# Kernel tuning notes

Measured on AMD Instinct MI355X. Metric: run time of the kernel, lower is better.

The kernel has to match this reference:

```python
import jax, jax.numpy as jnp
import numpy as np

B, T, C, H = 4, 2048, 1024, 16
D = C // H          # head_dim = 64
FF = 2 * C          # ff_mult = 2
EPS = 1e-5


def _layernorm(x, g, b):
    mu = jnp.mean(x, axis=-1, keepdims=True)
    var = jnp.mean((x - mu) ** 2, axis=-1, keepdims=True)
    return (x - mu) * jax.lax.rsqrt(var + EPS) * g + b


def setup_inputs() -> dict:
    key = jax.random.key(0)
    ks = jax.random.split(key, 8)
    x = jax.random.normal(ks[0], (B, T, C), dtype=jnp.float32)
    perm = jax.random.permutation(ks[1], T).astype(jnp.int32)
    s_c = 1.0 / np.sqrt(C)
    s_f = 1.0 / np.sqrt(FF)
    Wqkv = jax.random.normal(ks[2], (C, 3 * C), dtype=jnp.float32) * s_c
    Wproj = jax.random.normal(ks[3], (C, C), dtype=jnp.float32) * s_c
    bproj = jnp.zeros((C,), dtype=jnp.float32)
    ln1_g = jnp.ones((C,), dtype=jnp.float32)
    ln1_b = jnp.zeros((C,), dtype=jnp.float32)
    ln2_g = jnp.ones((C,), dtype=jnp.float32)
    ln2_b = jnp.zeros((C,), dtype=jnp.float32)
    Wff1 = jax.random.normal(ks[4], (C, FF), dtype=jnp.float32) * s_c
    bff1 = jnp.zeros((FF,), dtype=jnp.float32)
    Wff2 = jax.random.normal(ks[5], (FF, C), dtype=jnp.float32) * s_f
    bff2 = jnp.zeros((C,), dtype=jnp.float32)
    return {"x": x, "perm": perm, "Wqkv": Wqkv, "Wproj": Wproj, "bproj": bproj,
            "ln1_g": ln1_g, "ln1_b": ln1_b, "ln2_g": ln2_g, "ln2_b": ln2_b,
            "Wff1": Wff1, "bff1": bff1, "Wff2": Wff2, "bff2": bff2}


def reference(x, perm, Wqkv, Wproj, bproj, ln1_g, ln1_b, ln2_g, ln2_b,
              Wff1, bff1, Wff2, bff2):
    # --- attention branch ---
    h = _layernorm(x, ln1_g, ln1_b)                       # [B,T,C]
    qkv = (h @ Wqkv).reshape(B, T, 3, H, D)
    q, k, v = qkv[:, :, 0], qkv[:, :, 1], qkv[:, :, 2]    # [B,T,H,D]
    # random-permuted causal additive mask: masked = ~tril[:, perm]
    rows = jnp.arange(T)[:, None]
    masked = perm[None, :] > rows                          # [T,T] bool
    bias = jnp.where(masked, -jnp.inf, 0.0).astype(x.dtype)
    scale = 1.0 / np.sqrt(D)
    scores = jnp.einsum('bqhd,bkhd->bhqk', q, k) * scale + bias
    attn = jax.nn.softmax(scores, axis=-1)                 # [B,H,T,T]
    y = jnp.einsum('bhqk,bkhd->bqhd', attn, v).reshape(B, T, C)
    x = x + y @ Wproj + bproj
    # --- MLP branch ---
    h2 = _layernorm(x, ln2_g, ln2_b)
    ff = jax.nn.gelu(h2 @ Wff1 + bff1, approximate=False) @ Wff2 + bff2
    return x + ff
```

## Files before the change

kernel.cpp:

```cpp
#include <hip/hip_runtime.h>
#include <math.h>

#define Bb 4
#define Tt 2048
#define Cc 1024
#define Hh 16
#define Dd 64
#define FFf 2048
#define Mrows (Bb*Tt)

typedef _Float16 f16;
typedef _Float16 half8 __attribute__((ext_vector_type(8)));
typedef _Float16 half4 __attribute__((ext_vector_type(4)));
typedef _Float16 half2 __attribute__((ext_vector_type(2)));
typedef float floatx4 __attribute__((ext_vector_type(4)));
typedef float floatx16 __attribute__((ext_vector_type(16)));

#define MFMA16(a,b,c)    __builtin_amdgcn_mfma_f32_16x16x32_f16(a,b,c,0,0,0)
#define MFMA16K16(a,b,c) __builtin_amdgcn_mfma_f32_16x16x16f16(a,b,c,0,0,0)
#define MFMA32(a,b,c)    __builtin_amdgcn_mfma_f32_32x32x16_f16(a,b,c,0,0,0)

__device__ __forceinline__ void g2l16(const void* g, void* l) {
  __builtin_amdgcn_global_load_lds((__attribute__((address_space(1))) void*)(g),
                                   (__attribute__((address_space(3))) void*)(l),
                                   16, 0, 0);
}

__global__ __launch_bounds__(256) void wt_ln_kernel(
    const float* __restrict__ Wqkv, const float* __restrict__ Wproj,
    const float* __restrict__ Wff1, const float* __restrict__ Wff2,
    f16* __restrict__ WqkvT, f16* __restrict__ WprojT,
    f16* __restrict__ Wff1T, f16* __restrict__ Wff2T,
    const float* __restrict__ x, const float* __restrict__ gam,
    const float* __restrict__ bet, f16* __restrict__ lnout,
    const int* __restrict__ perm, int* __restrict__ inv) {
  const int tid = threadIdx.x;
  if (blockIdx.x >= 16384) {
    #pragma unroll
    for (int i = tid; i < Tt; i += 256) inv[perm[i]] = i;
    return;
  }
  if (blockIdx.x < 8192) {
    __shared__ float tile[32][33];
    int idx = blockIdx.x;
    const float* W; f16* WT; int K, N, n0, k0;
    if (idx < 3072)      { W = Wqkv;  WT = WqkvT;  K = Cc;  N = 3*Cc; n0 = (idx % 96)*32; k0 = (idx / 96)*32; }
    else if (idx < 4096) { idx -= 3072; W = Wproj; WT = WprojT; K = Cc;  N = Cc;  n0 = (idx % 32)*32; k0 = (idx / 32)*32; }
    else if (idx < 6144) { idx -= 4096; W = Wff1;  WT = Wff1T;  K = Cc;  N = FFf; n0 = (idx % 64)*32; k0 = (idx / 64)*32; }
    else                 { idx -= 6144; W = Wff2;  WT = Wff2T;  K = FFf; N = Cc;  n0 = (idx % 32)*32; k0 = (idx / 32)*32; }
    const int tx = tid & 31, ty = tid >> 5;
    #pragma unroll
    for (int i = 0; i < 4; i++)
      tile[ty + 8*i][tx] = W[(size_t)(k0 + ty + 8*i) * N + n0 + tx];
    __syncthreads();
    #pragma unroll
    for (int i = 0; i < 4; i++)
      WT[(size_t)(n0 + ty + 8*i) * K + k0 + tx] = (f16)tile[tx][ty + 8*i];
  } else {
    const int row = blockIdx.x - 8192;
    const float4 v = ((const float4*)(x + (size_t)row * Cc))[tid];
    float s  = v.x + v.y + v.z + v.w;
    float ss = v.x*v.x + v.y*v.y + v.z*v.z + v.w*v.w;
    #pragma unroll
    for (int o = 32; o >= 1; o >>= 1) { s += __shfl_xor(s, o); ss += __shfl_xor(ss, o); }
    __shared__ float ps[4], pss[4];
    if ((tid & 63) == 0) { ps[tid >> 6] = s; pss[tid >> 6] = ss; }
    __syncthreads();
    s  = ps[0] + ps[1] + ps[2] + ps[3];
    ss = pss[0] + pss[1] + pss[2] + pss[3];
    const float mu   = s * (1.0f / Cc);
    const float rstd = rsqrtf(ss * (1.0f / Cc) - mu * mu + 1e-5f);
    const float4 g4 = ((const float4*)gam)[tid];
    const float4 b4 = ((const float4*)bet)[tid];
    half4 o;
    o[0] = (f16)((v.x - mu) * rstd * g4.x + b4.x);
    o[1] = (f16)((v.y - mu) * rstd * g4.y + b4.y);
    o[2] = (f16)((v.z - mu) * rstd * g4.z + b4.z);
    o[3] = (f16)((v.w - mu) * rstd * g4.w + b4.w);
    ((half4*)(lnout + (size_t)row * Cc))[tid] = o;
  }
}

__global__ __launch_bounds__(256) void ln_kernel(const float* __restrict__ x,
                                                 const float* __restrict__ gam,
                                                 const float* __restrict__ bet,
                                                 f16* __restrict__ out) {
  const int row = blockIdx.x;
  const int tid = threadIdx.x;
  const float4 v = ((const float4*)(x + (size_t)row * Cc))[tid];
  float s  = v.x + v.y + v.z + v.w;
  float ss = v.x*v.x + v.y*v.y + v.z*v.z + v.w*v.w;
  #pragma unroll
  for (int o = 32; o >= 1; o >>= 1) { s += __shfl_xor(s, o); ss += __shfl_xor(ss, o); }
  __shared__ float ps[4], pss[4];
  if ((tid & 63) == 0) { ps[tid >> 6] = s; pss[tid >> 6] = ss; }
  __syncthreads();
  s  = ps[0] + ps[1] + ps[2] + ps[3];
  ss = pss[0] + pss[1] + pss[2] + pss[3];
  const float mu   = s * (1.0f / Cc);
  const float rstd = rsqrtf(ss * (1.0f / Cc) - mu * mu + 1e-5f);
  const float4 g4 = ((const float4*)gam)[tid];
  const float4 b4 = ((const float4*)bet)[tid];
  half4 o;
  o[0] = (f16)((v.x - mu) * rstd * g4.x + b4.x);
  o[1] = (f16)((v.y - mu) * rstd * g4.y + b4.y);
  o[2] = (f16)((v.z - mu) * rstd * g4.z + b4.z);
  o[3] = (f16)((v.w - mu) * rstd * g4.w + b4.w);
  ((half4*)(out + (size_t)row * Cc))[tid] = o;
}

template <int MODE>
__device__ __forceinline__ void gemm_epilogue_tile(
    const floatx16& a, int rowBase, int col, int khalf,
    const float* __restrict__ resid, const float* __restrict__ bias,
    float* __restrict__ outF, f16* __restrict__ outH,
    f16* __restrict__ outQ, f16* __restrict__ outK, f16* __restrict__ outV) {
  if (MODE == 0) {
    const int s = col >> 10;
    const int hh = (col >> 6) & 15;
    const int d = col & 63;
    #pragma unroll
    for (int g = 0; g < 4; g++) {
      const int row0 = rowBase + 4*khalf + 8*g;
      const int bI = row0 >> 11;
      const int t0 = row0 & 2047;
      if (s == 2) {
        const size_t addr = (((size_t)(bI*Hh + hh)) * Dd + d) * Tt +
                            (t0 & ~63) + ((t0 >> 2) & 3)*16 + ((t0 >> 4) & 3)*4;
        half4 o;
        #pragma unroll
        for (int r = 0; r < 4; r++) o[r] = (f16)a[g*4 + r];
        *(half4*)&outV[addr] = o;
      } else {
        f16* dst = (s == 0) ? outQ : outK;
        const float sc = (s == 0) ? 0.18033688f : 1.0f;
        #pragma unroll
        for (int r = 0; r < 4; r++)
          dst[(((size_t)(bI*Hh + hh)) * Tt + t0 + r) * Dd + d] = (f16)(a[g*4 + r] * sc);
      }
    }
  } else {
    #pragma unroll
    for (int g = 0; g < 4; g++) {
      #pragma unroll
      for (int r = 0; r < 4; r++) {
        const int row = rowBase + 4*khalf + 8*g + r;
        const float vv = a[g*4 + r];
        if (MODE == 1) {
          const size_t ad = (size_t)row * Cc + col;
          outF[ad] = vv + resid[ad] + bias[col];
        } else if (MODE == 2) {
          const float t = vv + bias[col];
          const float gl = 0.5f * t * (1.0f + erff(t * 0.70710678118654752f));
          outH[(size_t)row * FFf + col] = (f16)gl;
        } else {
          const size_t ad = (size_t)row * Cc + col;
          outF[ad] = vv + bias[col] + resid[ad];
        }
      }
    }
  }
}

template <int MODE>
__global__ __launch_bounds__(256, 4) void gemm_kernel(
    const f16* __restrict__ A, const f16* __restrict__ Bt, const int Kdim,
    const float* __restrict__ resid, const float* __restrict__ bias,
    float* __restrict__ outF, f16* __restrict__ outH,
    f16* __restrict__ outQ, f16* __restrict__ outK, f16* __restrict__ outV,
    const int* __restrict__ inv) {
  __shared__ f16 As[128 * 64];
  __shared__ f16 Bs[128 * 64];
  const int tid = threadIdx.x;
  const int lane = tid & 63;
  const int w = tid >> 6;
  const int wr = w >> 1, wc = w & 1;

  const int fid = blockIdx.y * gridDim.x + blockIdx.x;
  const int xcd = fid & 7;
  const int s = fid >> 3;
  const int r = s & 63;
  const int bm = xcd * 8 + (r >> 3);
  const int bn = (s >> 6) * 8 + (r & 7);

  floatx16 acc[2][2] = {};

  const int srow = lane >> 3;
  const int scol = ((lane & 7) ^ srow) * 8;
  size_t aRow[4];
  {
    const int r0 = bm*128 + w*32 + srow;
    if (MODE == 0 && bn >= 8) {
      const int bI = r0 >> 11;
      const int t0 = r0 & 2047;
      #pragma unroll
      for (int c = 0; c < 4; c++)
        aRow[c] = (size_t)(bI*Tt + inv[t0 + c*8]) * Kdim + scol;
    } else {
      #pragma unroll
      for (int c = 0; c < 4; c++)
        aRow[c] = (size_t)(r0 + c*8) * Kdim + scol;
    }
  }
  const size_t bBase = (size_t)(bn*128 + w*32 + srow) * Kdim + scol;

  const int m0 = wr*64 + (lane & 31);
  const int n0 = wc*64 + (lane & 31);
  const int khalf = lane >> 5;
  const int mx = (lane & 7);

  for (int ks = 0; ks < Kdim; ks += 64) {
    __syncthreads();
    #pragma unroll
    for (int c = 0; c < 4; c++) {
      g2l16(A  + aRow[c] + ks, &As[(w*32 + c*8) * 64]);
      g2l16(Bt + bBase + (size_t)(c*8)*Kdim + ks, &Bs[(w*32 + c*8) * 64]);
    }
    __syncthreads();
    #pragma unroll
    for (int kk = 0; kk < 4; kk++) {
      const int kg = kk*2 + khalf;
      half8 aF[2], bF[2];
      aF[0] = *(const half8*)&As[(m0     ) * 64 + ((kg ^ mx) * 8)];
      aF[1] = *(const half8*)&As[(m0 + 32) * 64 + ((kg ^ mx) * 8)];
      bF[0] = *(const half8*)&Bs[(n0     ) * 64 + ((kg ^ mx) * 8)];
      bF[1] = *(const half8*)&Bs[(n0 + 32) * 64 + ((kg ^ mx) * 8)];
      acc[0][0] = MFMA32(aF[0], bF[0], acc[0][0]);
      acc[0][1] = MFMA32(aF[0], bF[1], acc[0][1]);
      acc[1][0] = MFMA32(aF[1], bF[0], acc[1][0]);
      acc[1][1] = MFMA32(aF[1], bF[1], acc[1][1]);
    }
  }

  #pragma unroll
  for (int mi = 0; mi < 2; mi++)
    #pragma unroll
    for (int ni = 0; ni < 2; ni++)
      gemm_epilogue_tile<MODE>(acc[mi][ni], bm*128 + wr*64 + mi*32,
                               bn*128 + wc*64 + ni*32 + (lane & 31), khalf,
                               resid, bias, outF, outH, outQ, outK, outV);
}

__global__ __launch_bounds__(256, 4) void attn_kernel(
    const f16* __restrict__ Q, const f16* __restrict__ Kg,
    const f16* __restrict__ Vtp, f16* __restrict__ Y) {
  __shared__ f16 Ks[64 * 64];
  __shared__ f16 Vs[64 * 64];

  const int tid = threadIdx.x;
  const int lane = tid & 63;
  const int w = tid >> 6;
  const int low = lane & 15;
  const int quad = lane >> 4;
  const int bh = blockIdx.x;
  const int y = blockIdx.y;
  const int b = bh >> 4, h = bh & 15;

  const half4 ones4 = {(f16)1.f, (f16)1.f, (f16)1.f, (f16)1.f};
  const int gd = ((lane & 7) ^ (lane >> 3)) * 8;
  const int krow = lane >> 3;

  for (int pi = 0; pi < 2; pi++) {
    const int tile = (pi == 0) ? y : 15 - y;
    const int q0 = tile * 128;

    half8 qF[2][2];
    {
      const size_t base = ((size_t)bh * Tt + q0 + w*32) * Dd;
      #pragma unroll
      for (int qi = 0; qi < 2; qi++)
        #pragma unroll
        for (int kc = 0; kc < 2; kc++)
          qF[qi][kc] = *(const half8*)(Q + base + (size_t)(qi*16 + low) * Dd +
                                       kc*32 + quad*8);
    }

    floatx4 O[4][2] = {};
    floatx4 Ol[2] = {};
    const int nkb = (q0 >> 6) + 2;

    for (int kt = 0; kt < nkb; kt++) {
      const int kbase = kt * 64;
      __syncthreads();
      {
        const size_t kgBase = ((size_t)bh * Tt + kbase) * Dd;
        const size_t vgBase = ((size_t)bh * Dd) * Tt + kbase;
        g2l16(Kg  + kgBase + (size_t)(w*16 + 0 + krow) * Dd + gd, &Ks[(w*2 + 0) * 512]);
        g2l16(Kg  + kgBase + (size_t)(w*16 + 8 + krow) * Dd + gd, &Ks[(w*2 + 1) * 512]);
        g2l16(Vtp + vgBase + (size_t)(w*16 + 0 + krow) * Tt + gd, &Vs[(w*2 + 0) * 512]);
        g2l16(Vtp + vgBase + (size_t)(w*16 + 8 + krow) * Tt + gd, &Vs[(w*2 + 1) * 512]);
      }
      __syncthreads();

      floatx4 S[2][4] = {};
      #pragma unroll
      for (int kc = 0; kc < 2; kc++) {
        #pragma unroll
        for (int ki = 0; ki < 4; ki++) {
          const int key = ki*16 + low;
          const half8 kf = *(const half8*)&Ks[key * 64 + (((kc*4 + quad) ^ (lane & 7)) * 8)];
          S[0][ki] = MFMA16(kf, qF[0][kc], S[0][ki]);
          S[1][ki] = MFMA16(kf, qF[1][kc], S[1][ki]);
        }
      }

      half4 pF[2][4];
      const bool needmask = (kbase + 63 > q0 + w*32);
      if (needmask) {
        #pragma unroll
        for (int qi = 0; qi < 2; qi++) {
          const int qrow = q0 + w*32 + qi*16 + low;
          #pragma unroll
          for (int ki = 0; ki < 4; ki++) {
            const floatx4 sv = S[qi][ki];
            const int kj = kbase + ki*16 + quad*4;
            const float p0 = (kj + 0 > qrow) ? 0.f : __builtin_amdgcn_exp2f(sv[0]);
            const float p1 = (kj + 1 > qrow) ? 0.f : __builtin_amdgcn_exp2f(sv[1]);
            const float p2 = (kj + 2 > qrow) ? 0.f : __builtin_amdgcn_exp2f(sv[2]);
            const float p3 = (kj + 3 > qrow) ? 0.f : __builtin_amdgcn_exp2f(sv[3]);
            const half2 lo = __builtin_bit_cast(half2, __builtin_amdgcn_cvt_pkrtz(p0, p1));
            const half2 hi = __builtin_bit_cast(half2, __builtin_amdgcn_cvt_pkrtz(p2, p3));
            pF[qi][ki] = __builtin_shufflevector(lo, hi, 0, 1, 2, 3);
          }
        }
      } else {
        #pragma unroll
        for (int qi = 0; qi < 2; qi++) {
          #pragma unroll
          for (int ki = 0; ki < 4; ki++) {
            const floatx4 sv = S[qi][ki];
            const float p0 = __builtin_amdgcn_exp2f(sv[0]);
            const float p1 = __builtin_amdgcn_exp2f(sv[1]);
            const float p2 = __builtin_amdgcn_exp2f(sv[2]);
            const float p3 = __builtin_amdgcn_exp2f(sv[3]);
            const half2 lo = __builtin_bit_cast(half2, __builtin_amdgcn_cvt_pkrtz(p0, p1));
            const half2 hi = __builtin_bit_cast(half2, __builtin_amdgcn_cvt_pkrtz(p2, p3));
            pF[qi][ki] = __builtin_shufflevector(lo, hi, 0, 1, 2, 3);
          }
        }
      }

      #pragma unroll
      for (int ki2 = 0; ki2 < 2; ki2++) {
        Ol[0] = MFMA16K16(ones4, pF[0][2*ki2 + 0], Ol[0]);
        Ol[1] = MFMA16K16(ones4, pF[1][2*ki2 + 0], Ol[1]);
        Ol[0] = MFMA16K16(ones4, pF[0][2*ki2 + 1], Ol[0]);
        Ol[1] = MFMA16K16(ones4, pF[1][2*ki2 + 1], Ol[1]);
        #pragma unroll
        for (int ni = 0; ni < 4; ni++) {
          const int d = ni*16 + low;
          const half8 v8 = *(const half8*)&Vs[d * 64 + (((quad*2 + ki2) ^ (lane & 7)) * 8)];
          const half4 vfA = __builtin_shufflevector(v8, v8, 0, 1, 2, 3);
          const half4 vfB = __builtin_shufflevector(v8, v8, 4, 5, 6, 7);
          O[ni][0] = MFMA16K16(vfA, pF[0][2*ki2 + 0], O[ni][0]);
          O[ni][1] = MFMA16K16(vfA, pF[1][2*ki2 + 0], O[ni][1]);
          O[ni][0] = MFMA16K16(vfB, pF[0][2*ki2 + 1], O[ni][0]);
          O[ni][1] = MFMA16K16(vfB, pF[1][2*ki2 + 1], O[ni][1]);
        }
      }
    }

    #pragma unroll
    for (int qi = 0; qi < 2; qi++) {
      const float linv = 1.0f / Ol[qi][0];
      const int trow = q0 + w*32 + qi*16 + low;
      #pragma unroll
      for (int ni = 0; ni < 4; ni++) {
        half4 o;
        #pragma unroll
        for (int rr = 0; rr < 4; rr++) o[rr] = (f16)(O[ni][qi][rr] * linv);
        *(half4*)&Y[((size_t)(b * Tt + trow)) * Cc + h*64 + ni*16 + quad*4] = o;
      }
    }
  }
}

extern "C" void kernel_launch(void* const* d_in, const int* in_sizes, int n_in,
                              void* d_out, int out_size, void* d_ws, size_t ws_size,
                              hipStream_t stream) {
  const float* x     = (const float*)d_in[0];
  const int*   perm  = (const int*)d_in[1];
  const float* Wqkv  = (const float*)d_in[2];
  const float* Wproj = (const float*)d_in[3];
  const float* bproj = (const float*)d_in[4];
  const float* ln1g  = (const float*)d_in[5];
  const float* ln1b  = (const float*)d_in[6];
  const float* ln2g  = (const float*)d_in[7];
  const float* ln2b  = (const float*)d_in[8];
  const float* Wff1  = (const float*)d_in[9];
  const float* bff1  = (const float*)d_in[10];
  const float* Wff2  = (const float*)d_in[11];
  const float* bff2  = (const float*)d_in[12];
  float* out = (float*)d_out;

  char* ws = (char*)d_ws;
  size_t off = 0;
  auto alloc = [&](size_t bytes) -> void* {
    void* p = ws + off;
    off += (bytes + 255) & ~(size_t)255;
    return p;
  };
  f16*   h1     = (f16*)alloc((size_t)Mrows * Cc * 2);
  f16*   qb     = (f16*)alloc((size_t)Mrows * Cc * 2);
  f16*   kb     = (f16*)alloc((size_t)Mrows * Cc * 2);
  f16*   vtp    = (f16*)alloc((size_t)Mrows * Cc * 2);
  f16*   yb     = (f16*)alloc((size_t)Mrows * Cc * 2);
  float* xa     = (float*)alloc((size_t)Mrows * Cc * 4);
  f16*   h2     = (f16*)alloc((size_t)Mrows * Cc * 2);
  f16*   gb     = (f16*)alloc((size_t)Mrows * FFf * 2);
  f16*   WqkvT  = (f16*)alloc((size_t)3 * Cc * Cc * 2);
  f16*   WprojT = (f16*)alloc((size_t)Cc * Cc * 2);
  f16*   Wff1T  = (f16*)alloc((size_t)FFf * Cc * 2);
  f16*   Wff2T  = (f16*)alloc((size_t)Cc * FFf * 2);
  int*   inv    = (int*)alloc((size_t)Tt * 4);

  wt_ln_kernel<<<16385, 256, 0, stream>>>(Wqkv, Wproj, Wff1, Wff2,
                                          WqkvT, WprojT, Wff1T, Wff2T,
                                          x, ln1g, ln1b, h1, perm, inv);

  gemm_kernel<0><<<dim3(3*Cc/128, Mrows/128), 256, 0, stream>>>(
      h1, WqkvT, Cc, nullptr, nullptr, nullptr, nullptr, qb, kb, vtp, inv);

  attn_kernel<<<dim3(Bb*Hh, Tt/256), 256, 0, stream>>>(qb, kb, vtp, yb);

  gemm_kernel<1><<<dim3(Cc/128, Mrows/128), 256, 0, stream>>>(
      yb, WprojT, Cc, x, bproj, xa, nullptr, nullptr, nullptr, nullptr, nullptr);

  ln_kernel<<<Mrows, 256, 0, stream>>>(xa, ln2g, ln2b, h2);

  gemm_kernel<2><<<dim3(FFf/128, Mrows/128), 256, 0, stream>>>(
      h2, Wff1T, Cc, nullptr, bff1, nullptr, gb, nullptr, nullptr, nullptr, nullptr);

  gemm_kernel<3><<<dim3(Cc/128, Mrows/128), 256, 0, stream>>>(
      gb, Wff2T, FFf, xa, bff2, out, nullptr, nullptr, nullptr, nullptr, nullptr);
}
```

Measured before the change: 407.2 us.

## Split attention query tile across 8 waves with 16 rows each

The attention kernel now launches 512 threads (8 waves) per block instead of 256. Each wave owns 16 query rows instead of 32, and each wave loads one 8-row K/V slab into shared memory instead of two. This raises the number of waves available to hide MFMA, exp and LDS latency and cuts per-wave register use. In exchange, each LDS K/V fragment is reused for half as many MFMAs per wave, and barrier cost grows with more waves per block.

```diff
diff --git a/kernel.cpp b/kernel.cpp
--- a/kernel.cpp
+++ b/kernel.cpp
@@ -241,7 +241,7 @@
                                resid, bias, outF, outH, outQ, outK, outV);
 }
 
-__global__ __launch_bounds__(256, 4) void attn_kernel(
+__global__ __launch_bounds__(512, 4) void attn_kernel(
     const f16* __restrict__ Q, const f16* __restrict__ Kg,
     const f16* __restrict__ Vtp, f16* __restrict__ Y) {
   __shared__ f16 Ks[64 * 64];
@@ -264,19 +264,16 @@
     const int tile = (pi == 0) ? y : 15 - y;
     const int q0 = tile * 128;
 
-    half8 qF[2][2];
+    half8 qF[2];
     {
-      const size_t base = ((size_t)bh * Tt + q0 + w*32) * Dd;
-      #pragma unroll
-      for (int qi = 0; qi < 2; qi++)
-        #pragma unroll
-        for (int kc = 0; kc < 2; kc++)
-          qF[qi][kc] = *(const half8*)(Q + base + (size_t)(qi*16 + low) * Dd +
-                                       kc*32 + quad*8);
-    }
-
-    floatx4 O[4][2] = {};
-    floatx4 Ol[2] = {};
+      const size_t base = ((size_t)bh * Tt + q0 + w*16) * Dd;
+      #pragma unroll
+      for (int kc = 0; kc < 2; kc++)
+        qF[kc] = *(const half8*)(Q + base + (size_t)low * Dd + kc*32 + quad*8);
+    }
+
+    floatx4 O[4] = {};
+    floatx4 Ol = {};
     const int nkb = (q0 >> 6) + 2;
 
     for (int kt = 0; kt < nkb; kt++) {
@@ -285,90 +282,76 @@
       {
         const size_t kgBase = ((size_t)bh * Tt + kbase) * Dd;
         const size_t vgBase = ((size_t)bh * Dd) * Tt + kbase;
-        g2l16(Kg  + kgBase + (size_t)(w*16 + 0 + krow) * Dd + gd, &Ks[(w*2 + 0) * 512]);
-        g2l16(Kg  + kgBase + (size_t)(w*16 + 8 + krow) * Dd + gd, &Ks[(w*2 + 1) * 512]);
-        g2l16(Vtp + vgBase + (size_t)(w*16 + 0 + krow) * Tt + gd, &Vs[(w*2 + 0) * 512]);
-        g2l16(Vtp + vgBase + (size_t)(w*16 + 8 + krow) * Tt + gd, &Vs[(w*2 + 1) * 512]);
+        g2l16(Kg  + kgBase + (size_t)(w*8 + krow) * Dd + gd, &Ks[w * 512]);
+        g2l16(Vtp + vgBase + (size_t)(w*8 + krow) * Tt + gd, &Vs[w * 512]);
       }
       __syncthreads();
 
-      floatx4 S[2][4] = {};
+      floatx4 S[4] = {};
       #pragma unroll
       for (int kc = 0; kc < 2; kc++) {
         #pragma unroll
         for (int ki = 0; ki < 4; ki++) {
           const int key = ki*16 + low;
           const half8 kf = *(const half8*)&Ks[key * 64 + (((kc*4 + quad) ^ (lane & 7)) * 8)];
-          S[0][ki] = MFMA16(kf, qF[0][kc], S[0][ki]);
-          S[1][ki] = MFMA16(kf, qF[1][kc], S[1][ki]);
+          S[ki] = MFMA16(kf, qF[kc], S[ki]);
         }
       }
 
-      half4 pF[2][4];
-      const bool needmask = (kbase + 63 > q0 + w*32);
+      half4 pF[4];
+      const bool needmask = (kbase + 63 > q0 + w*16);
       if (needmask) {
-        #pragma unroll
-        for (int qi = 0; qi < 2; qi++) {
-          const int qrow = q0 + w*32 + qi*16 + low;
-          #pragma unroll
-          for (int ki = 0; ki < 4; ki++) {
-            const floatx4 sv = S[qi][ki];
-            const int kj = kbase + ki*16 + quad*4;
-            const float p0 = (kj + 0 > qrow) ? 0.f : __builtin_amdgcn_exp2f(sv[0]);
-            const float p1 = (kj + 1 > qrow) ? 0.f : __builtin_amdgcn_exp2f(sv[1]);
-            const float p2 = (kj + 2 > qrow) ? 0.f : __builtin_amdgcn_exp2f(sv[2]);
-            const float p3 = (kj + 3 > qrow) ? 0.f : __builtin_amdgcn_exp2f(sv[3]);
-            const half2 lo = __builtin_bit_cast(half2, __builtin_amdgcn_cvt_pkrtz(p0, p1));
-            const half2 hi = __builtin_bit_cast(half2, __builtin_amdgcn_cvt_pkrtz(p2, p3));
-            pF[qi][ki] = __builtin_shufflevector(lo, hi, 0, 1, 2, 3);
-          }
+        const int qrow = q0 + w*16 + low;
+        #pragma unroll
+        for (int ki = 0; ki < 4; ki++) {
+          const floatx4 sv = S[ki];
+          const int kj = kbase + ki*16 + quad*4;
+          const float p0 = (kj + 0 > qrow) ? 0.f : __builtin_amdgcn_exp2f(sv[0]);
+          const float p1 = (kj + 1 > qrow) ? 0.f : __builtin_amdgcn_exp2f(sv[1]);
+          const float p2 = (kj + 2 > qrow) ? 0.f : __builtin_amdgcn_exp2f(sv[2]);
+          const float p3 = (kj + 3 > qrow) ? 0.f : __builtin_amdgcn_exp2f(sv[3]);
+          const half2 lo = __builtin_bit_cast(half2, __builtin_amdgcn_cvt_pkrtz(p0, p1));
+          const half2 hi = __builtin_bit_cast(half2, __builtin_amdgcn_cvt_pkrtz(p2, p3));
+          pF[ki] = __builtin_shufflevector(lo, hi, 0, 1, 2, 3);
         }
       } else {
         #pragma unroll
-        for (int qi = 0; qi < 2; qi++) {
-          #pragma unroll
-          for (int ki = 0; ki < 4; ki++) {
-            const floatx4 sv = S[qi][ki];
-            const float p0 = __builtin_amdgcn_exp2f(sv[0]);
-            const float p1 = __builtin_amdgcn_exp2f(sv[1]);
-            const float p2 = __builtin_amdgcn_exp2f(sv[2]);
-            const float p3 = __builtin_amdgcn_exp2f(sv[3]);
-            const half2 lo = __builtin_bit_cast(half2, __builtin_amdgcn_cvt_pkrtz(p0, p1));
-            const half2 hi = __builtin_bit_cast(half2, __builtin_amdgcn_cvt_pkrtz(p2, p3));
-            pF[qi][ki] = __builtin_shufflevector(lo, hi, 0, 1, 2, 3);
-          }
+        for (int ki = 0; ki < 4; ki++) {
+          const floatx4 sv = S[ki];
+          const float p0 = __builtin_amdgcn_exp2f(sv[0]);
+          const float p1 = __builtin_amdgcn_exp2f(sv[1]);
+          const float p2 = __builtin_amdgcn_exp2f(sv[2]);
+          const float p3 = __builtin_amdgcn_exp2f(sv[3]);
+          const half2 lo = __builtin_bit_cast(half2, __builtin_amdgcn_cvt_pkrtz(p0, p1));
+          const half2 hi = __builtin_bit_cast(half2, __builtin_amdgcn_cvt_pkrtz(p2, p3));
+          pF[ki] = __builtin_shufflevector(lo, hi, 0, 1, 2, 3);
         }
       }
 
       #pragma unroll
       for (int ki2 = 0; ki2 < 2; ki2++) {
-        Ol[0] = MFMA16K16(ones4, pF[0][2*ki2 + 0], Ol[0]);
-        Ol[1] = MFMA16K16(ones4, pF[1][2*ki2 + 0], Ol[1]);
-        Ol[0] = MFMA16K16(ones4, pF[0][2*ki2 + 1], Ol[0]);
-        Ol[1] = MFMA16K16(ones4, pF[1][2*ki2 + 1], Ol[1]);
+        Ol = MFMA16K16(ones4, pF[2*ki2 + 0], Ol);
+        Ol = MFMA16K16(ones4, pF[2*ki2 + 1], Ol);
         #pragma unroll
         for (int ni = 0; ni < 4; ni++) {
           const int d = ni*16 + low;
           const half8 v8 = *(const half8*)&Vs[d * 64 + (((quad*2 + ki2) ^ (lane & 7)) * 8)];
           const half4 vfA = __builtin_shufflevector(v8, v8, 0, 1, 2, 3);
           const half4 vfB = __builtin_shufflevector(v8, v8, 4, 5, 6, 7);
-          O[ni][0] = MFMA16K16(vfA, pF[0][2*ki2 + 0], O[ni][0]);
-          O[ni][1] = MFMA16K16(vfA, pF[1][2*ki2 + 0], O[ni][1]);
-          O[ni][0] = MFMA16K16(vfB, pF[0][2*ki2 + 1], O[ni][0]);
-          O[ni][1] = MFMA16K16(vfB, pF[1][2*ki2 + 1], O[ni][1]);
+          O[ni] = MFMA16K16(vfA, pF[2*ki2 + 0], O[ni]);
+          O[ni] = MFMA16K16(vfB, pF[2*ki2 + 1], O[ni]);
         }
       }
     }
 
-    #pragma unroll
-    for (int qi = 0; qi < 2; qi++) {
-      const float linv = 1.0f / Ol[qi][0];
-      const int trow = q0 + w*32 + qi*16 + low;
+    {
+      const float linv = 1.0f / Ol[0];
+      const int trow = q0 + w*16 + low;
       #pragma unroll
       for (int ni = 0; ni < 4; ni++) {
         half4 o;
         #pragma unroll
-        for (int rr = 0; rr < 4; rr++) o[rr] = (f16)(O[ni][qi][rr] * linv);
+        for (int rr = 0; rr < 4; rr++) o[rr] = (f16)(O[ni][rr] * linv);
         *(half4*)&Y[((size_t)(b * Tt + trow)) * Cc + h*64 + ni*16 + quad*4] = o;
       }
     }
@@ -421,7 +404,7 @@
   gemm_kernel<0><<<dim3(3*Cc/128, Mrows/128), 256, 0, stream>>>(
       h1, WqkvT, Cc, nullptr, nullptr, nullptr, nullptr, qb, kb, vtp, inv);
 
-  attn_kernel<<<dim3(Bb*Hh, Tt/256), 256, 0, stream>>>(qb, kb, vtp, yb);
+  attn_kernel<<<dim3(Bb*Hh, Tt/256), 512, 0, stream>>>(qb, kb, vtp, yb);
 
   gemm_kernel<1><<<dim3(Cc/128, Mrows/128), 256, 0, stream>>>(
       yb, WprojT, Cc, x, bproj, xa, nullptr, nullptr, nullptr, nullptr, nullptr);
```

Result: no change. 402.1 us (-1.2%).
